# Performance work log

Hardware: AMD Instinct MI355X
Metric: run time of the kernel (lower is better)

## Reference

```python
import jax, jax.numpy as jnp
import numpy as np

B, D = 32768, 512
DEPTH = 7
ORDERS = (1, 2, 3, 5)
COUPLING_STRENGTH = 1.0


def _damping_coeffs():
    # frequency_dependent profile: 0.1 / (1 + exp(linspace(0, 3, D)))
    freqs = jnp.exp(jnp.linspace(0.0, 3.0, D))
    return 0.1 / (1.0 + freqs)


def _generate_harmonics(wave, hmats):
    acc = jnp.zeros_like(wave)
    for order, H in zip(ORDERS, hmats):
        hw = wave @ H.astype(wave.dtype)
        if order == 1:
            h = hw
        elif order == 2:
            h = hw * jnp.conj(hw)
        elif order == 3:
            h = hw * jnp.conj(hw) * hw
        else:
            mag = jnp.abs(hw)
            ph = jnp.angle(hw)
            h = (mag ** (1.0 / order)) * jnp.exp(1j * (ph * float(order)))
        acc = acc + h * (1.0 / (order * order))
    return acc


def _nonlinearity(wave, scale, bias):
    re = jnp.tanh(wave.real * scale + bias)
    im = jnp.tanh(wave.imag * scale + bias)
    return jax.lax.complex(re, im)


def _forward(wave_real, wave_imag, coupling_matrix, harmonic_1, harmonic_2,
             harmonic_3, harmonic_5, mixing_scale, mixing_bias):
    wave = jax.lax.complex(wave_real, wave_imag)  # [B, D] complex64
    hmats = (harmonic_1, harmonic_2, harmonic_3, harmonic_5)
    damping = _damping_coeffs()  # [D], non-trainable constant

    chamber = wave
    history = []
    for depth in range(DEPTH):
        transformed = (chamber @ coupling_matrix.astype(chamber.dtype)) * COUPLING_STRENGTH
        with_harmonics = transformed + _generate_harmonics(chamber, hmats)
        if depth > 0:
            # InterferenceLayer approximated as complex wave superposition
            interference = chamber + with_harmonics
        else:
            interference = with_harmonics
        nl = _nonlinearity(interference, mixing_scale, mixing_bias)
        factor = jnp.exp(-damping * float(depth)).astype(jnp.float32)
        chamber = nl * factor.astype(nl.dtype)
        history.append(chamber)

    w = jnp.exp(-jnp.linspace(0.0, 2.0, DEPTH))
    w = w / jnp.sum(w)
    stacked = jnp.stack(history)  # [DEPTH, B, D]
    out = jnp.sum(stacked * w[:, None, None].astype(stacked.dtype), axis=0)
    return out


def setup_inputs() -> dict:
    key = jax.random.key(0)
    ks = jax.random.split(key, 8)
    s = 1.0 / np.sqrt(D)  # approx orthogonal init scale
    return {
        "wave_real": jax.random.normal(ks[0], (B, D), jnp.float32),
        "wave_imag": jax.random.normal(ks[1], (B, D), jnp.float32),
        "coupling_matrix": jax.random.normal(ks[2], (D, D), jnp.float32) * s,
        "harmonic_1": jax.random.normal(ks[3], (D, D), jnp.float32) * s,
        "harmonic_2": jax.random.normal(ks[4], (D, D), jnp.float32) * s,
        "harmonic_3": jax.random.normal(ks[5], (D, D), jnp.float32) * s,
        "harmonic_5": jax.random.normal(ks[6], (D, D), jnp.float32) * s,
        "mixing_scale": jnp.ones((D,), jnp.float32),
        "mixing_bias": jnp.zeros((D,), jnp.float32),
    }


def reference(wave_real, wave_imag, coupling_matrix, harmonic_1, harmonic_2,
              harmonic_3, harmonic_5, mixing_scale, mixing_bias):
    out = _forward(wave_real, wave_imag, coupling_matrix, harmonic_1,
                   harmonic_2, harmonic_3, harmonic_5, mixing_scale, mixing_bias)
    # return as stacked real/imag float32 [2, B, D] for harness comparability
    return jnp.stack([out.real, out.imag])
```

## Files before the change

### kernel.cpp

```cpp
#include <hip/hip_runtime.h>
#include <hip/hip_bf16.h>
#include <cstdint>


typedef __bf16 bf16_t;
typedef bf16_t bf16x8 __attribute__((ext_vector_type(8)));
typedef float f32x4 __attribute__((ext_vector_type(4)));
typedef _Float16 h2_t __attribute__((ext_vector_type(2)));

#define B_ROWS 32768
#define D_DIM 512
#define N_DEPTH 7
#define BD ((size_t)B_ROWS * D_DIM)

__device__ __forceinline__ unsigned short f2b(float f) {
  bf16_t h = (bf16_t)f;
  return __builtin_bit_cast(unsigned short, h);
}
__device__ __forceinline__ float b2f(unsigned short u) {
  bf16_t h = __builtin_bit_cast(bf16_t, u);
  return (float)h;
}
__device__ __forceinline__ float fast_tanh(float x) {
  float ax = fabsf(x);
  float e = __expf(2.0f * ax);
  float t = 1.0f - 2.0f / (e + 1.0f);
  return copysignf(t, x);
}
__device__ __forceinline__ int lds_addr(int row, int byte_in_row) {
  return row * 1024 + (byte_in_row ^ ((row & 7) << 4));
}

__global__ __launch_bounds__(256) void prepack_v2(
    const float* __restrict__ cm, const float* __restrict__ h1,
    const float* __restrict__ h2, const float* __restrict__ h3,
    const float* __restrict__ h5, unsigned short* __restrict__ dst) {
  int gid = blockIdx.x * 256 + threadIdx.x;
  if (gid >= 32 * 16 * 64) return;
  int l  = gid & 63;
  int ks = (gid >> 6) & 15;
  int t  = gid >> 10;
  int n  = t * 16 + (l & 15);
  int k0 = ks * 32 + (l >> 4) * 8;
  unsigned short* base = dst + ((size_t)(t * 16 + ks) * 6) * 512 + l * 8;
  bf16x8 f0, f1, f2, f3, f4, f5;
#pragma unroll
  for (int i = 0; i < 8; ++i) {
    size_t idx = (size_t)(k0 + i) * D_DIM + n;
    float v0 = cm[idx] + h1[idx];
    unsigned short h0 = f2b(v0);
    f0[i] = __builtin_bit_cast(bf16_t, h0);
    f1[i] = (bf16_t)(v0 - b2f(h0));
    f2[i] = (bf16_t)h2[idx];
    f3[i] = (bf16_t)h3[idx];
    float v5 = h5[idx];
    unsigned short h5v = f2b(v5);
    f4[i] = __builtin_bit_cast(bf16_t, h5v);
    f5[i] = (bf16_t)(v5 - b2f(h5v));
  }
  *(bf16x8*)(base + 0 * 512) = f0;
  *(bf16x8*)(base + 1 * 512) = f1;
  *(bf16x8*)(base + 2 * 512) = f2;
  *(bf16x8*)(base + 3 * 512) = f3;
  *(bf16x8*)(base + 4 * 512) = f4;
  *(bf16x8*)(base + 5 * 512) = f5;
}

__global__ __launch_bounds__(1024) void resonance_kernel(
    const float* __restrict__ wr, const float* __restrict__ wi,
    const float* __restrict__ scale, const float* __restrict__ bias,
    const unsigned short* __restrict__ pre, float* __restrict__ out) {
  __shared__ unsigned short lds_hi[32 * 512];
  __shared__ unsigned short lds_lo[32 * 512];

  const int tid  = threadIdx.x;
  const int lane = tid & 63;
  const int wave = tid >> 6;
  const int ln15 = lane & 15;
  const int lg   = lane >> 4;
  const int r0   = blockIdx.x * 16;

#pragma unroll
  for (int it = 0; it < 2; ++it) {
    int idx = it * 1024 + tid;
    int row = idx >> 6;
    int k0  = (idx & 63) * 8;
    const float* src = (row < 16)
        ? (wr + (size_t)(r0 + row) * D_DIM + k0)
        : (wi + (size_t)(r0 + row - 16) * D_DIM + k0);
    float4 v0 = *(const float4*)(src);
    float4 v1 = *(const float4*)(src + 4);
    float v[8] = {v0.x, v0.y, v0.z, v0.w, v1.x, v1.y, v1.z, v1.w};
    bf16x8 ph, pl;
#pragma unroll
    for (int j = 0; j < 8; ++j) {
      unsigned short h = f2b(v[j]);
      ph[j] = __builtin_bit_cast(bf16_t, h);
      pl[j] = (bf16_t)(v[j] - b2f(h));
    }
    int ad = lds_addr(row, k0 * 2);
    *(bf16x8*)((char*)lds_hi + ad) = ph;
    *(bf16x8*)((char*)lds_lo + ad) = pl;
  }
  __syncthreads();

  float Wsum = 0.0f;
#pragma unroll
  for (int d = 0; d < N_DEPTH; ++d) Wsum += __expf(-(float)d * (1.0f / 3.0f));
  const float invW = 1.0f / Wsum;

  h2_t oacc[2][4];
  h2_t news[2][4];
#pragma unroll
  for (int c = 0; c < 2; ++c)
#pragma unroll
    for (int r = 0; r < 4; ++r) oacc[c][r] = (h2_t){(_Float16)0.f, (_Float16)0.f};

  for (int depth = 0; depth < N_DEPTH; ++depth) {
    const float wd = __expf(-(float)depth * (1.0f / 3.0f)) * invW;

#pragma unroll
    for (int c = 0; c < 2; ++c) {
      const int t = c * 16 + wave;
      f32x4 acc0[2], acc1[2], acc2[2], acc3[2];
#pragma unroll
      for (int mt = 0; mt < 2; ++mt) {
        acc0[mt] = (f32x4){0.f, 0.f, 0.f, 0.f};
        acc1[mt] = (f32x4){0.f, 0.f, 0.f, 0.f};
        acc2[mt] = (f32x4){0.f, 0.f, 0.f, 0.f};
        acc3[mt] = (f32x4){0.f, 0.f, 0.f, 0.f};
      }

      const unsigned short* bb = pre + ((size_t)(t * 16) * 6 + 3) * 512 + lane * 8;
#pragma unroll 2
      for (int ks = 0; ks < 16; ++ks) {
        bf16x8 ah[2], al[2];
#pragma unroll
        for (int mt = 0; mt < 2; ++mt) {
          int ad = lds_addr(mt * 16 + ln15, ks * 64 + lg * 16);
          ah[mt] = *(const bf16x8*)((const char*)lds_hi + ad);
          al[mt] = *(const bf16x8*)((const char*)lds_lo + ad);
        }
        bf16x8 b0h = *(const bf16x8*)(bb - 1536);
        bf16x8 b0l = *(const bf16x8*)(bb - 1024);
        bf16x8 b1h = *(const bf16x8*)(bb - 512);
        bf16x8 b2h = *(const bf16x8*)(bb);
        bf16x8 b3h = *(const bf16x8*)(bb + 512);
        bf16x8 b3l = *(const bf16x8*)(bb + 1024);
        bb += 3072;
#pragma unroll
        for (int mt = 0; mt < 2; ++mt) {
          acc0[mt] = __builtin_amdgcn_mfma_f32_16x16x32_bf16(ah[mt], b0h, acc0[mt], 0, 0, 0);
          acc0[mt] = __builtin_amdgcn_mfma_f32_16x16x32_bf16(al[mt], b0h, acc0[mt], 0, 0, 0);
          acc0[mt] = __builtin_amdgcn_mfma_f32_16x16x32_bf16(ah[mt], b0l, acc0[mt], 0, 0, 0);
          acc1[mt] = __builtin_amdgcn_mfma_f32_16x16x32_bf16(ah[mt], b1h, acc1[mt], 0, 0, 0);
          acc2[mt] = __builtin_amdgcn_mfma_f32_16x16x32_bf16(ah[mt], b2h, acc2[mt], 0, 0, 0);
          acc3[mt] = __builtin_amdgcn_mfma_f32_16x16x32_bf16(ah[mt], b3h, acc3[mt], 0, 0, 0);
          acc3[mt] = __builtin_amdgcn_mfma_f32_16x16x32_bf16(al[mt], b3h, acc3[mt], 0, 0, 0);
          acc3[mt] = __builtin_amdgcn_mfma_f32_16x16x32_bf16(ah[mt], b3l, acc3[mt], 0, 0, 0);
        }
      }

      const int col = t * 16 + ln15;
      const float sclv = scale[col];
      const float biav = bias[col];
      const float damp = 0.1f / (1.0f + __expf(3.0f * (float)col * (1.0f / 511.0f)));
      const float fac  = __expf(-damp * (float)depth);
#pragma unroll
      for (int r = 0; r < 4; ++r) {
        float lr = acc0[0][r],  li = acc0[1][r];
        float re2 = acc1[0][r], im2 = acc1[1][r];
        float ar = 0.25f * (re2 * re2 + im2 * im2);
        float re3 = acc2[0][r], im3 = acc2[1][r];
        float m3 = re3 * re3 + im3 * im3;
        ar += 0.111111111f * m3 * re3;
        float ai = 0.111111111f * m3 * im3;
        float re5 = acc3[0][r], im5 = acc3[1][r];
        float m5 = re5 * re5 + im5 * im5;
        {
          float m5c = fmaxf(m5, 1e-36f);
          float inv = rsqrtf(m5c);
          float ur = re5 * inv, ui = im5 * inv;
          float u2r = ur * ur - ui * ui,     u2i = 2.0f * ur * ui;
          float u4r = u2r * u2r - u2i * u2i, u4i = 2.0f * u2r * u2i;
          float u5r = u4r * ur - u4i * ui,   u5i = u4r * ui + u4i * ur;
          float mag = __expf(0.1f * __logf(m5c));
          float msk = (m5 > 1e-36f) ? 0.04f : 0.0f;
          ar += msk * mag * u5r;
          ai += msk * mag * u5i;
        }
        float ir = lr + ar, ii = li + ai;
        if (depth > 0) {
          ir += (float)news[c][r][0];
          ii += (float)news[c][r][1];
        }
        float cre = fast_tanh(ir * sclv + biav) * fac;
        float cim = fast_tanh(ii * sclv + biav) * fac;
        oacc[c][r] += (h2_t){(_Float16)(wd * cre), (_Float16)(wd * cim)};
        news[c][r] = (h2_t){(_Float16)cre, (_Float16)cim};
      }
    }

    if (depth < N_DEPTH - 1) {
      __syncthreads();
#pragma unroll
      for (int c = 0; c < 2; ++c) {
        const int colb = ((c * 16 + wave) * 16 + ln15) * 2;
#pragma unroll
        for (int r = 0; r < 4; ++r) {
          const int brow = lg * 4 + r;
          float cre = (float)news[c][r][0];
          float cim = (float)news[c][r][1];
          unsigned short hr = f2b(cre);
          unsigned short lr = f2b(cre - b2f(hr));
          unsigned short hi = f2b(cim);
          unsigned short li = f2b(cim - b2f(hi));
          int ar_ = lds_addr(brow, colb);
          int ai_ = lds_addr(brow + 16, colb);
          *(unsigned short*)((char*)lds_hi + ar_) = hr;
          *(unsigned short*)((char*)lds_lo + ar_) = lr;
          *(unsigned short*)((char*)lds_hi + ai_) = hi;
          *(unsigned short*)((char*)lds_lo + ai_) = li;
        }
      }
      __syncthreads();
    }
  }

#pragma unroll
  for (int c = 0; c < 2; ++c) {
    const int col = (c * 16 + wave) * 16 + ln15;
#pragma unroll
    for (int r = 0; r < 4; ++r) {
      int brow = lg * 4 + r;
      size_t base = (size_t)(r0 + brow) * D_DIM + col;
      out[base] = (float)oacc[c][r][0];
      out[BD + base] = (float)oacc[c][r][1];
    }
  }
}

extern "C" void kernel_launch(void* const* d_in, const int* in_sizes, int n_in,
                              void* d_out, int out_size, void* d_ws, size_t ws_size,
                              hipStream_t stream) {
  const float* wr = (const float*)d_in[0];
  const float* wi = (const float*)d_in[1];
  const float* cm = (const float*)d_in[2];
  const float* h1 = (const float*)d_in[3];
  const float* h2 = (const float*)d_in[4];
  const float* h3 = (const float*)d_in[5];
  const float* h5 = (const float*)d_in[6];
  const float* sc = (const float*)d_in[7];
  const float* bi = (const float*)d_in[8];
  unsigned short* pre = (unsigned short*)d_ws;
  float* out = (float*)d_out;

  hipLaunchKernelGGL(prepack_v2, dim3(128), dim3(256), 0, stream,
                     cm, h1, h2, h3, h5, pre);
  hipLaunchKernelGGL(resonance_kernel, dim3(B_ROWS / 16), dim3(1024), 0, stream,
                     wr, wi, sc, bi, pre, out);
}
```

Before: 2.366 ms.

## Double-buffer chamber state in LDS and drop one barrier per depth

The single LDS buffer holding the bf16 hi/lo split of the chamber becomes a ping-pong pair. Each wave writes the next state straight into the other buffer from its epilogue, so one __syncthreads per depth replaces the previous two plus a separate write-back loop. The residual chamber term is now read back from the bf16 hi+lo LDS copy instead of fp16 registers, which drops the news[] registers. The cost is twice the LDS per block (128KB), which may limit occupancy, plus extra LDS reads in the epilogue.

```diff
diff --git a/kernel.cpp b/kernel.cpp
--- a/kernel.cpp
+++ b/kernel.cpp
@@ -70,8 +70,8 @@
     const float* __restrict__ wr, const float* __restrict__ wi,
     const float* __restrict__ scale, const float* __restrict__ bias,
     const unsigned short* __restrict__ pre, float* __restrict__ out) {
-  __shared__ unsigned short lds_hi[32 * 512];
-  __shared__ unsigned short lds_lo[32 * 512];
+  __shared__ unsigned short lds_hi[2][32 * 512];
+  __shared__ unsigned short lds_lo[2][32 * 512];
 
   const int tid  = threadIdx.x;
   const int lane = tid & 63;
@@ -99,8 +99,8 @@
       pl[j] = (bf16_t)(v[j] - b2f(h));
     }
     int ad = lds_addr(row, k0 * 2);
-    *(bf16x8*)((char*)lds_hi + ad) = ph;
-    *(bf16x8*)((char*)lds_lo + ad) = pl;
+    *(bf16x8*)((char*)lds_hi[0] + ad) = ph;
+    *(bf16x8*)((char*)lds_lo[0] + ad) = pl;
   }
   __syncthreads();
 
@@ -110,14 +110,18 @@
   const float invW = 1.0f / Wsum;
 
   h2_t oacc[2][4];
-  h2_t news[2][4];
 #pragma unroll
   for (int c = 0; c < 2; ++c)
 #pragma unroll
     for (int r = 0; r < 4; ++r) oacc[c][r] = (h2_t){(_Float16)0.f, (_Float16)0.f};
 
+  int cur = 0;
   for (int depth = 0; depth < N_DEPTH; ++depth) {
     const float wd = __expf(-(float)depth * (1.0f / 3.0f)) * invW;
+    const char* Ahi = (const char*)lds_hi[cur];
+    const char* Alo = (const char*)lds_lo[cur];
+    char* Nhi = (char*)lds_hi[cur ^ 1];
+    char* Nlo = (char*)lds_lo[cur ^ 1];
 
 #pragma unroll
     for (int c = 0; c < 2; ++c) {
@@ -138,8 +142,8 @@
 #pragma unroll
         for (int mt = 0; mt < 2; ++mt) {
           int ad = lds_addr(mt * 16 + ln15, ks * 64 + lg * 16);
-          ah[mt] = *(const bf16x8*)((const char*)lds_hi + ad);
-          al[mt] = *(const bf16x8*)((const char*)lds_lo + ad);
+          ah[mt] = *(const bf16x8*)(Ahi + ad);
+          al[mt] = *(const bf16x8*)(Alo + ad);
         }
         bf16x8 b0h = *(const bf16x8*)(bb - 1536);
         bf16x8 b0l = *(const bf16x8*)(bb - 1024);
@@ -168,6 +172,7 @@
       const float fac  = __expf(-damp * (float)depth);
 #pragma unroll
       for (int r = 0; r < 4; ++r) {
+        const int brow = lg * 4 + r;
         float lr = acc0[0][r],  li = acc0[1][r];
         float re2 = acc1[0][r], im2 = acc1[1][r];
         float ar = 0.25f * (re2 * re2 + im2 * im2);
@@ -190,41 +195,30 @@
           ai += msk * mag * u5i;
         }
         float ir = lr + ar, ii = li + ai;
+        const int colb = col * 2;
+        const int ar_ = lds_addr(brow, colb);
+        const int ai_ = lds_addr(brow + 16, colb);
         if (depth > 0) {
-          ir += (float)news[c][r][0];
-          ii += (float)news[c][r][1];
+          ir += b2f(*(const unsigned short*)(Ahi + ar_))
+              + b2f(*(const unsigned short*)(Alo + ar_));
+          ii += b2f(*(const unsigned short*)(Ahi + ai_))
+              + b2f(*(const unsigned short*)(Alo + ai_));
         }
         float cre = fast_tanh(ir * sclv + biav) * fac;
         float cim = fast_tanh(ii * sclv + biav) * fac;
         oacc[c][r] += (h2_t){(_Float16)(wd * cre), (_Float16)(wd * cim)};
-        news[c][r] = (h2_t){(_Float16)cre, (_Float16)cim};
+        if (depth < N_DEPTH - 1) {
+          unsigned short hr = f2b(cre);
+          unsigned short hi = f2b(cim);
+          *(unsigned short*)(Nhi + ar_) = hr;
+          *(unsigned short*)(Nlo + ar_) = f2b(cre - b2f(hr));
+          *(unsigned short*)(Nhi + ai_) = hi;
+          *(unsigned short*)(Nlo + ai_) = f2b(cim - b2f(hi));
+        }
       }
     }
-
-    if (depth < N_DEPTH - 1) {
-      __syncthreads();
-#pragma unroll
-      for (int c = 0; c < 2; ++c) {
-        const int colb = ((c * 16 + wave) * 16 + ln15) * 2;
-#pragma unroll
-        for (int r = 0; r < 4; ++r) {
-          const int brow = lg * 4 + r;
-          float cre = (float)news[c][r][0];
-          float cim = (float)news[c][r][1];
-          unsigned short hr = f2b(cre);
-          unsigned short lr = f2b(cre - b2f(hr));
-          unsigned short hi = f2b(cim);
-          unsigned short li = f2b(cim - b2f(hi));
-          int ar_ = lds_addr(brow, colb);
-          int ai_ = lds_addr(brow + 16, colb);
-          *(unsigned short*)((char*)lds_hi + ar_) = hr;
-          *(unsigned short*)((char*)lds_lo + ar_) = lr;
-          *(unsigned short*)((char*)lds_hi + ai_) = hi;
-          *(unsigned short*)((char*)lds_lo + ai_) = li;
-        }
-      }
-      __syncthreads();
-    }
+    __syncthreads();
+    cur ^= 1;
   }
 
 #pragma unroll
```

New measurement: 1.946 ms. 17.7% less time.
